# Kernel optimization log

Measured on AMD Instinct MI355X. Metric: run time of the kernel, lower is better.

## Reference

```python
import jax, jax.numpy as jnp
import numpy as np

N_NODES = 100000
N_EDGES = 1600000
VOCAB = 2048
NODE_DIM = 64
HIDDEN = 64
N_MASK = 10000


def setup_inputs() -> dict:
    key = jax.random.key(0)
    ks = jax.random.split(key, 10)
    x = jax.random.randint(ks[0], (N_NODES, 1), 0, VOCAB, dtype=jnp.int64)
    edge_index = jax.random.randint(ks[1], (2, N_EDGES), 0, N_NODES, dtype=jnp.int64)
    mask_x_position = jax.random.randint(ks[2], (N_MASK,), 0, N_NODES, dtype=jnp.int64)
    # embedding init: normal with std = node_dim ** -0.5 (as in initialize_parameters)
    emb = jax.random.normal(ks[3], (VOCAB, NODE_DIM), dtype=jnp.float32) * (NODE_DIM ** -0.5)
    # SAGEConv layer 1: lin_l (neighbors, with bias), lin_r (root, no bias)
    s1 = (NODE_DIM ** -0.5)
    W_l1 = jax.random.uniform(ks[4], (NODE_DIM, HIDDEN), jnp.float32, -s1, s1)
    b_l1 = jnp.zeros((HIDDEN,), jnp.float32)
    W_r1 = jax.random.uniform(ks[5], (NODE_DIM, HIDDEN), jnp.float32, -s1, s1)
    # SAGEConv layer 2
    s2 = (HIDDEN ** -0.5)
    W_l2 = jax.random.uniform(ks[6], (HIDDEN, VOCAB), jnp.float32, -s2, s2)
    b_l2 = jnp.zeros((VOCAB,), jnp.float32)
    W_r2 = jax.random.uniform(ks[7], (HIDDEN, VOCAB), jnp.float32, -s2, s2)
    return {"x": x, "edge_index": edge_index, "mask_x_position": mask_x_position,
            "emb": emb, "W_l1": W_l1, "b_l1": b_l1, "W_r1": W_r1,
            "W_l2": W_l2, "b_l2": b_l2, "W_r2": W_r2}


def _sage_conv(h, src, dst, W_l, b_l, W_r):
    # mean-aggregate source-node features at destination nodes (PyG SAGEConv, aggr='mean')
    msgs = h[src]                                                  # [E, D]
    agg = jax.ops.segment_sum(msgs, dst, num_segments=N_NODES)     # [N, D]
    deg = jax.ops.segment_sum(jnp.ones((src.shape[0], 1), h.dtype), dst,
                              num_segments=N_NODES)                # [N, 1]
    mean = agg / jnp.maximum(deg, 1.0)
    return mean @ W_l + b_l + h @ W_r


def reference(x, edge_index, mask_x_position, emb, W_l1, b_l1, W_r1, W_l2, b_l2, W_r2):
    src, dst = edge_index[0], edge_index[1]
    h = emb[x[:, 0]]                                # embedding(x).squeeze(1) -> [N, node_dim]
    # dropout is identity in eval mode
    h = _sage_conv(h, src, dst, W_l1, b_l1, W_r1)   # [N, hidden]
    h = jax.nn.relu(h)
    h = _sage_conv(h, src, dst, W_l2, b_l2, W_r2)   # [N, vocab]
    return jax.nn.log_softmax(h[mask_x_position], axis=1)
```

## Files before the change

kernel.cpp:

```cpp
#include <hip/hip_runtime.h>
#include <math.h>

#define N_NODES   100000
#define N_EDGES   1600000
#define VOCAB     2048
#define NODE_DIM  64
#define HIDDEN    64
#define N_MASK    10000

#define BN        192
#define NBKT      521
#define CHUNK     4096
#define NCH       391

typedef __attribute__((ext_vector_type(8))) short short8;
typedef __attribute__((ext_vector_type(4))) float f32x4;
typedef unsigned short ushort_t;
typedef unsigned int uint_t;

#define H1_OFF      0
#define ESRC_OFF    25600000
#define EVOC_OFF    32000000
#define E2_OFF      38400000
#define EWL_OFF     38400000
#define EWR_OFF     38924288
#define W2T_OFF     39448576
#define X2B_OFF     39972864
#define ROWPTR_OFF  51200000
#define BCNT_OFF    51600016
#define BPTR_OFF    51602112
#define BCUR_OFF    51604208

__device__ __forceinline__ ushort_t f2bf(float f) {
    uint_t u = __builtin_bit_cast(uint_t, f);
    u += 0x7FFFu + ((u >> 16) & 1u);
    return (ushort_t)(u >> 16);
}

__global__ __launch_bounds__(256) void k_prep(const float* __restrict__ emb,
                                              const float* __restrict__ Wl1,
                                              const float* __restrict__ Wr1,
                                              const float* __restrict__ Wl2,
                                              const float* __restrict__ Wr2,
                                              float* __restrict__ embWl,
                                              float* __restrict__ embWr,
                                              ushort_t* __restrict__ W2T) {
    __shared__ ushort_t T[64 * 66];
    const int bx = blockIdx.x;
    const int tid = threadIdx.x;
    if (bx < 1024) {
        const int half = bx >> 9;
        const float* W = half ? Wr1 : Wl1;
        float* out = half ? embWr : embWl;
        int idx = (bx & 511) * 256 + tid;
        int v = idx >> 6, c = idx & 63;
        float s = 0.0f;
#pragma unroll 8
        for (int k = 0; k < 64; k++) s += emb[v * 64 + k] * W[k * 64 + c];
        out[idx] = s;
    } else {
        int t = bx - 1024;
        const int k0 = (t & 1) * 64;
        const int n0 = (t >> 1) * 64;
        const float* Wsrc = (k0 == 0) ? Wl2 : Wr2;
#pragma unroll
        for (int i = 0; i < 16; i++) {
            int idx = i * 256 + tid;
            int k = idx >> 6, n = idx & 63;
            T[n * 66 + k] = f2bf(Wsrc[(size_t)k * VOCAB + n0 + n]);
        }
        __syncthreads();
#pragma unroll
        for (int i = 0; i < 16; i++) {
            int idx = i * 256 + tid;
            int n = idx >> 6, k = idx & 63;
            W2T[(size_t)(n0 + n) * 128 + k0 + k] = T[n * 66 + k];
        }
    }
}

__global__ __launch_bounds__(256) void k_count(const int* __restrict__ dst,
                                               int* __restrict__ bcnt) {
    __shared__ int hist[NBKT];
    for (int i = threadIdx.x; i < NBKT; i += 256) hist[i] = 0;
    __syncthreads();
    int stride = gridDim.x * 256;
    for (int e = blockIdx.x * 256 + threadIdx.x; e < N_EDGES; e += stride)
        atomicAdd(&hist[dst[e] / BN], 1);
    __syncthreads();
    for (int i = threadIdx.x; i < NBKT; i += 256) {
        int c = hist[i];
        if (c) atomicAdd(&bcnt[i], c);
    }
}

__global__ __launch_bounds__(1024) void k_bscan(const int* __restrict__ bcnt,
                                                int* __restrict__ bptr,
                                                int* __restrict__ bcur,
                                                int* __restrict__ rowptr) {
    __shared__ int s[1024];
    int t = threadIdx.x;
    int v = (t < NBKT) ? bcnt[t] : 0;
    s[t] = v;
    __syncthreads();
    for (int off = 1; off < 1024; off <<= 1) {
        int a = (t >= off) ? s[t - off] : 0;
        __syncthreads();
        s[t] += a;
        __syncthreads();
    }
    if (t < NBKT) { bptr[t] = s[t] - v; bcur[t] = s[t] - v; }
    if (t == NBKT - 1) bptr[NBKT] = s[t];
    if (t == 0) rowptr[N_NODES] = N_EDGES;
}

__global__ __launch_bounds__(256) void k_scatter2(const int* __restrict__ src,
                                                  const int* __restrict__ dst,
                                                  const int* __restrict__ x,
                                                  int* __restrict__ bcur,
                                                  int2* __restrict__ e2) {
    __shared__ uint_t dstb[CHUNK];
    __shared__ int hist[NBKT];
    const int e0 = blockIdx.x * CHUNK;
    const int n = min(CHUNK, N_EDGES - e0);
    for (int i = threadIdx.x; i < NBKT; i += 256) hist[i] = 0;
    __syncthreads();
    for (int i = threadIdx.x; i < n; i += 256) {
        int d = dst[e0 + i];
        int b = d / BN;
        dstb[i] = ((uint_t)b << 8) | (uint_t)(d - b * BN);
        atomicAdd(&hist[b], 1);
    }
    __syncthreads();
    for (int i = threadIdx.x; i < NBKT; i += 256) {
        int c = hist[i];
        hist[i] = c ? atomicAdd(&bcur[i], c) : 0;
    }
    __syncthreads();
    for (int i = threadIdx.x; i < n; i += 256) {
        uint_t db = dstb[i];
        int b = db >> 8;
        int s = src[e0 + i];
        int voc = x[s];
        int pos = atomicAdd(&hist[b], 1);
        e2[pos] = make_int2(s, (voc << 8) | (int)(db & 255u));
    }
}

__global__ __launch_bounds__(256) void k_sortb(const int* __restrict__ bptr,
                                               const int2* __restrict__ e2,
                                               int* __restrict__ rowptr,
                                               int* __restrict__ esrc,
                                               int* __restrict__ evoc) {
    __shared__ int cnt[BN];
    __shared__ int s[256];
    __shared__ int cur[BN];
    const int b = blockIdx.x;
    const int t = threadIdx.x;
    const int r0 = bptr[b], r1 = bptr[b + 1];
    if (t < BN) cnt[t] = 0;
    __syncthreads();
    for (int e = r0 + t; e < r1; e += 256)
        atomicAdd(&cnt[e2[e].y & 255], 1);
    __syncthreads();
    int v = (t < BN) ? cnt[t] : 0;
    s[t] = v;
    __syncthreads();
    for (int off = 1; off < 256; off <<= 1) {
        int a = (t >= off) ? s[t - off] : 0;
        __syncthreads();
        s[t] += a;
        __syncthreads();
    }
    if (t < BN) {
        int excl = s[t] - v;
        cur[t] = excl;
        int node = b * BN + t;
        if (node < N_NODES) rowptr[node] = r0 + excl;
    }
    __syncthreads();
    for (int e = r0 + t; e < r1; e += 256) {
        int2 ev = e2[e];
        int pos = r0 + atomicAdd(&cur[ev.y & 255], 1);
        esrc[pos] = ev.x;
        evoc[pos] = ev.y >> 8;
    }
}

__global__ __launch_bounds__(256) void k_agg1(const int* __restrict__ rowptr,
                                              const int* __restrict__ evoc,
                                              const int* __restrict__ x,
                                              const float* __restrict__ embWl,
                                              const float* __restrict__ embWr,
                                              const float* __restrict__ b1,
                                              float* __restrict__ h1) {
    int gw = (blockIdx.x * 256 + threadIdx.x) >> 6;
    int lane = threadIdx.x & 63;
    if (gw >= N_NODES) return;
    int r0 = rowptr[gw], r1 = rowptr[gw + 1];
    int deg = r1 - r0;
    float s0 = 0.0f, s1 = 0.0f, s2 = 0.0f, s3 = 0.0f;
    for (int base = 0; base < deg; base += 64) {
        int cnt = min(64, deg - base);
        int myv = (base + lane < deg) ? evoc[r0 + base + lane] : 0;
        int t = 0;
        for (; t + 3 < cnt; t += 4) {
            int va = __shfl(myv, t);
            int vb = __shfl(myv, t + 1);
            int vc = __shfl(myv, t + 2);
            int vd = __shfl(myv, t + 3);
            s0 += embWl[(va << 6) + lane];
            s1 += embWl[(vb << 6) + lane];
            s2 += embWl[(vc << 6) + lane];
            s3 += embWl[(vd << 6) + lane];
        }
        for (; t < cnt; t++)
            s0 += embWl[(__shfl(myv, t) << 6) + lane];
    }
    float sum = (s0 + s1) + (s2 + s3);
    float inv = 1.0f / fmaxf((float)deg, 1.0f);
    float self = embWr[(x[gw] << 6) + lane];
    h1[((size_t)gw << 6) + lane] = fmaxf(sum * inv + self + b1[lane], 0.0f);
}

__global__ __launch_bounds__(256) void k_x2(const int* __restrict__ mask,
                                            const int* __restrict__ rowptr,
                                            const int* __restrict__ esrc,
                                            const float* __restrict__ h1,
                                            ushort_t* __restrict__ X2b) {
    int gw = (blockIdx.x * 256 + threadIdx.x) >> 6;
    int lane = threadIdx.x & 63;
    if (gw >= N_MASK) return;
    int n = mask[gw];
    int r0 = rowptr[n], r1 = rowptr[n + 1];
    int deg = r1 - r0;
    float s0 = 0.0f, s1 = 0.0f, s2 = 0.0f, s3 = 0.0f;
    for (int base = 0; base < deg; base += 64) {
        int cnt = min(64, deg - base);
        int mys = (base + lane < deg) ? esrc[r0 + base + lane] : 0;
        int t = 0;
        for (; t + 3 < cnt; t += 4) {
            int sa = __shfl(mys, t);
            int sb = __shfl(mys, t + 1);
            int sc = __shfl(mys, t + 2);
            int sd = __shfl(mys, t + 3);
            s0 += h1[((size_t)sa << 6) + lane];
            s1 += h1[((size_t)sb << 6) + lane];
            s2 += h1[((size_t)sc << 6) + lane];
            s3 += h1[((size_t)sd << 6) + lane];
        }
        for (; t < cnt; t++)
            s0 += h1[((size_t)__shfl(mys, t) << 6) + lane];
    }
    float sum = (s0 + s1) + (s2 + s3);
    float inv = 1.0f / fmaxf((float)deg, 1.0f);
    X2b[gw * 128 + lane]      = f2bf(sum * inv);
    X2b[gw * 128 + 64 + lane] = f2bf(h1[((size_t)n << 6) + lane]);
}

__global__ __launch_bounds__(256) void k_gemm2_mfma(const ushort_t* __restrict__ X2b,
                                                    const ushort_t* __restrict__ W2T,
                                                    const float* __restrict__ bias,
                                                    float* __restrict__ out,
                                                    int M) {
    __shared__ ushort_t As[64 * 144];
    __shared__ ushort_t Bs[64 * 144];
    const int tid  = threadIdx.x;
    const int row0 = blockIdx.x * 64;
    const int col0 = blockIdx.y * 64;

#pragma unroll
    for (int i = 0; i < 4; i++) {
        int idx = i * 256 + tid;
        int r = idx >> 4, ch = idx & 15;
        int R = row0 + r;
        short8 v = {0, 0, 0, 0, 0, 0, 0, 0};
        if (R < M) v = *(const short8*)(X2b + (size_t)R * 128 + ch * 8);
        *(short8*)(As + r * 144 + ch * 8) = v;
    }
#pragma unroll
    for (int i = 0; i < 4; i++) {
        int idx = i * 256 + tid;
        int r = idx >> 4, ch = idx & 15;
        *(short8*)(Bs + r * 144 + ch * 8) =
            *(const short8*)(W2T + (size_t)(col0 + r) * 128 + ch * 8);
    }
    __syncthreads();

    const int lane = tid & 63;
    const int wv   = tid >> 6;
    const int wr = wv >> 1, wc = wv & 1;
    const int l15 = lane & 15, q = lane >> 4;

    f32x4 acc[2][2] = {};
    const ushort_t* Abase = As + (wr * 32 + l15) * 144 + q * 8;
    const ushort_t* Bbase = Bs + (wc * 32 + l15) * 144 + q * 8;

#pragma unroll
    for (int ks = 0; ks < 4; ks++) {
        short8 a0 = *(const short8*)(Abase + ks * 32);
        short8 a1 = *(const short8*)(Abase + 16 * 144 + ks * 32);
        short8 b0 = *(const short8*)(Bbase + ks * 32);
        short8 b1 = *(const short8*)(Bbase + 16 * 144 + ks * 32);
        acc[0][0] = __builtin_amdgcn_mfma_f32_16x16x32_bf16(a0, b0, acc[0][0], 0, 0, 0);
        acc[0][1] = __builtin_amdgcn_mfma_f32_16x16x32_bf16(a0, b1, acc[0][1], 0, 0, 0);
        acc[1][0] = __builtin_amdgcn_mfma_f32_16x16x32_bf16(a1, b0, acc[1][0], 0, 0, 0);
        acc[1][1] = __builtin_amdgcn_mfma_f32_16x16x32_bf16(a1, b1, acc[1][1], 0, 0, 0);
    }

#pragma unroll
    for (int ni = 0; ni < 2; ni++) {
        int c_ = col0 + wc * 32 + ni * 16 + l15;
        float bv = bias[c_];
#pragma unroll
        for (int mi = 0; mi < 2; mi++) {
#pragma unroll
            for (int reg = 0; reg < 4; reg++) {
                int r_ = row0 + wr * 32 + mi * 16 + q * 4 + reg;
                if (r_ < M) out[(size_t)r_ * VOCAB + c_] = acc[mi][ni][reg] + bv;
            }
        }
    }
}

__global__ __launch_bounds__(256) void k_logsoftmax(float* __restrict__ out) {
    const int row = blockIdx.x;
    float4* p4 = (float4*)(out + (size_t)row * VOCAB);
    const int tid = threadIdx.x;
    float4 v[2];
    float m = -INFINITY;
#pragma unroll
    for (int i = 0; i < 2; i++) {
        v[i] = p4[tid + i * 256];
        m = fmaxf(m, fmaxf(fmaxf(v[i].x, v[i].y), fmaxf(v[i].z, v[i].w)));
    }
#pragma unroll
    for (int off = 1; off < 64; off <<= 1) m = fmaxf(m, __shfl_xor(m, off));
    __shared__ float redm[4];
    __shared__ float reds[4];
    int wave = tid >> 6;
    if ((tid & 63) == 0) redm[wave] = m;
    __syncthreads();
    m = fmaxf(fmaxf(redm[0], redm[1]), fmaxf(redm[2], redm[3]));
    float s = 0.0f;
#pragma unroll
    for (int i = 0; i < 2; i++)
        s += expf(v[i].x - m) + expf(v[i].y - m) + expf(v[i].z - m) + expf(v[i].w - m);
#pragma unroll
    for (int off = 1; off < 64; off <<= 1) s += __shfl_xor(s, off);
    if ((tid & 63) == 0) reds[wave] = s;
    __syncthreads();
    s = reds[0] + reds[1] + reds[2] + reds[3];
    float L = m + logf(s);
#pragma unroll
    for (int i = 0; i < 2; i++) {
        float4 o = v[i];
        o.x -= L; o.y -= L; o.z -= L; o.w -= L;
        p4[tid + i * 256] = o;
    }
}

extern "C" void kernel_launch(void* const* d_in, const int* in_sizes, int n_in,
                              void* d_out, int out_size, void* d_ws, size_t ws_size,
                              hipStream_t stream) {
    const int*   x    = (const int*)d_in[0];
    const int*   ei   = (const int*)d_in[1];
    const int*   src  = ei;
    const int*   dst  = ei + N_EDGES;
    const int*   mask = (const int*)d_in[2];
    const float* emb  = (const float*)d_in[3];
    const float* Wl1  = (const float*)d_in[4];
    const float* bl1  = (const float*)d_in[5];
    const float* Wr1  = (const float*)d_in[6];
    const float* Wl2  = (const float*)d_in[7];
    const float* bl2  = (const float*)d_in[8];
    const float* Wr2  = (const float*)d_in[9];
    float* out = (float*)d_out;

    char* ws = (char*)d_ws;
    float*    h1     = (float*)(ws + H1_OFF);
    int*      esrc   = (int*)(ws + ESRC_OFF);
    int*      evoc   = (int*)(ws + EVOC_OFF);
    int2*     e2     = (int2*)(ws + E2_OFF);
    float*    embWl  = (float*)(ws + EWL_OFF);
    float*    embWr  = (float*)(ws + EWR_OFF);
    ushort_t* W2T    = (ushort_t*)(ws + W2T_OFF);
    ushort_t* X2b    = (ushort_t*)(ws + X2B_OFF);
    int*      rowptr = (int*)(ws + ROWPTR_OFF);
    int*      bcnt   = (int*)(ws + BCNT_OFF);
    int*      bptr   = (int*)(ws + BPTR_OFF);
    int*      bcur   = (int*)(ws + BCUR_OFF);

    hipMemsetAsync(ws + BCNT_OFF, 0, 2096, stream);

    k_count   <<<512, 256, 0, stream>>>(dst, bcnt);
    k_bscan   <<<1, 1024, 0, stream>>>(bcnt, bptr, bcur, rowptr);
    k_scatter2<<<NCH, 256, 0, stream>>>(src, dst, x, bcur, e2);
    k_sortb   <<<NBKT, 256, 0, stream>>>(bptr, e2, rowptr, esrc, evoc);

    k_prep<<<1088, 256, 0, stream>>>(emb, Wl1, Wr1, Wl2, Wr2, embWl, embWr, W2T);

    k_agg1<<<(N_NODES * 64 + 255) / 256, 256, 0, stream>>>(rowptr, evoc, x, embWl, embWr, bl1, h1);

    k_x2<<<(N_MASK * 64 + 255) / 256, 256, 0, stream>>>(mask, rowptr, esrc, h1, X2b);
    dim3 g2((N_MASK + 63) / 64, VOCAB / 64);
    k_gemm2_mfma<<<g2, 256, 0, stream>>>(X2b, W2T, bl2, out, N_MASK);

    k_logsoftmax<<<N_MASK, 256, 0, stream>>>(out);
}
```

Before: 301.9 us.

## Fuse per-bucket sort with layer-1 aggregation using shared-memory edge lists

```diff
diff --git a/kernel.cpp b/kernel.cpp
--- a/kernel.cpp
+++ b/kernel.cpp
@@ -10,8 +10,9 @@
 
 #define BN        192
 #define NBKT      521
-#define CHUNK     4096
-#define NCH       391
+#define CHUNK     1024
+#define NCH       1563
+#define ELCAP     4096
 
 typedef __attribute__((ext_vector_type(8))) short short8;
 typedef __attribute__((ext_vector_type(4))) float f32x4;
@@ -20,16 +21,15 @@
 
 #define H1_OFF      0
 #define ESRC_OFF    25600000
-#define EVOC_OFF    32000000
-#define E2_OFF      38400000
-#define EWL_OFF     38400000
-#define EWR_OFF     38924288
-#define W2T_OFF     39448576
-#define X2B_OFF     39972864
-#define ROWPTR_OFF  51200000
-#define BCNT_OFF    51600016
-#define BPTR_OFF    51602112
-#define BCUR_OFF    51604208
+#define E2_OFF      32000000
+#define EWL_OFF     44800000
+#define EWR_OFF     45324288
+#define W2T_OFF     45848576
+#define X2B_OFF     46372864
+#define ROWPTR_OFF  48932864
+#define BCNT_OFF    49332880
+#define BPTR_OFF    49334976
+#define BCUR_OFF    49337072
 
 __device__ __forceinline__ ushort_t f2bf(float f) {
     uint_t u = __builtin_bit_cast(uint_t, f);
@@ -119,108 +119,114 @@
                                                   const int* __restrict__ x,
                                                   int* __restrict__ bcur,
                                                   int2* __restrict__ e2) {
-    __shared__ uint_t dstb[CHUNK];
     __shared__ int hist[NBKT];
     const int e0 = blockIdx.x * CHUNK;
     const int n = min(CHUNK, N_EDGES - e0);
-    for (int i = threadIdx.x; i < NBKT; i += 256) hist[i] = 0;
-    __syncthreads();
-    for (int i = threadIdx.x; i < n; i += 256) {
-        int d = dst[e0 + i];
-        int b = d / BN;
-        dstb[i] = ((uint_t)b << 8) | (uint_t)(d - b * BN);
-        atomicAdd(&hist[b], 1);
-    }
-    __syncthreads();
-    for (int i = threadIdx.x; i < NBKT; i += 256) {
+    const int tid = threadIdx.x;
+    for (int i = tid; i < NBKT; i += 256) hist[i] = 0;
+    __syncthreads();
+    int d[4], s[4], voc[4], bk[4];
+#pragma unroll
+    for (int i = 0; i < 4; i++) {
+        int idx = i * 256 + tid;
+        if (idx < n) {
+            d[i] = dst[e0 + idx];
+            s[i] = src[e0 + idx];
+            voc[i] = x[s[i]];
+            bk[i] = d[i] / BN;
+            atomicAdd(&hist[bk[i]], 1);
+        }
+    }
+    __syncthreads();
+    for (int i = tid; i < NBKT; i += 256) {
         int c = hist[i];
         hist[i] = c ? atomicAdd(&bcur[i], c) : 0;
     }
     __syncthreads();
-    for (int i = threadIdx.x; i < n; i += 256) {
-        uint_t db = dstb[i];
-        int b = db >> 8;
-        int s = src[e0 + i];
-        int voc = x[s];
-        int pos = atomicAdd(&hist[b], 1);
-        e2[pos] = make_int2(s, (voc << 8) | (int)(db & 255u));
-    }
-}
-
-__global__ __launch_bounds__(256) void k_sortb(const int* __restrict__ bptr,
-                                               const int2* __restrict__ e2,
-                                               int* __restrict__ rowptr,
-                                               int* __restrict__ esrc,
-                                               int* __restrict__ evoc) {
-    __shared__ int cnt[BN];
-    __shared__ int s[256];
+#pragma unroll
+    for (int i = 0; i < 4; i++) {
+        int idx = i * 256 + tid;
+        if (idx < n) {
+            int pos = atomicAdd(&hist[bk[i]], 1);
+            e2[pos] = make_int2(s[i], (voc[i] << 8) | (d[i] - bk[i] * BN));
+        }
+    }
+}
+
+__global__ __launch_bounds__(512) void k_sortagg(const int* __restrict__ bptr,
+                                                 const int2* __restrict__ e2,
+                                                 const int* __restrict__ x,
+                                                 const float* __restrict__ embWl,
+                                                 const float* __restrict__ embWr,
+                                                 const float* __restrict__ b1,
+                                                 int* __restrict__ rowptr,
+                                                 int* __restrict__ esrc,
+                                                 float* __restrict__ h1) {
+    __shared__ int2 eL[ELCAP];
+    __shared__ int sc[256];
     __shared__ int cur[BN];
+    __shared__ int base[BN + 1];
     const int b = blockIdx.x;
     const int t = threadIdx.x;
     const int r0 = bptr[b], r1 = bptr[b + 1];
-    if (t < BN) cnt[t] = 0;
-    __syncthreads();
-    for (int e = r0 + t; e < r1; e += 256)
-        atomicAdd(&cnt[e2[e].y & 255], 1);
-    __syncthreads();
-    int v = (t < BN) ? cnt[t] : 0;
-    s[t] = v;
-    __syncthreads();
+    const int m = r1 - r0;
+
+    if (t < 256) sc[t] = 0;
+    __syncthreads();
+    for (int i = t; i < m; i += 512)
+        atomicAdd(&sc[e2[r0 + i].y & 255], 1);
+    __syncthreads();
+    int v = (t < 256) ? sc[t] : 0;
     for (int off = 1; off < 256; off <<= 1) {
-        int a = (t >= off) ? s[t - off] : 0;
+        int a = (t >= off && t < 256) ? sc[t - off] : 0;
         __syncthreads();
-        s[t] += a;
+        if (t < 256) sc[t] += a;
         __syncthreads();
     }
     if (t < BN) {
-        int excl = s[t] - v;
+        int excl = sc[t] - v;
+        base[t] = excl;
         cur[t] = excl;
         int node = b * BN + t;
         if (node < N_NODES) rowptr[node] = r0 + excl;
-    }
-    __syncthreads();
-    for (int e = r0 + t; e < r1; e += 256) {
-        int2 ev = e2[e];
-        int pos = r0 + atomicAdd(&cur[ev.y & 255], 1);
-        esrc[pos] = ev.x;
-        evoc[pos] = ev.y >> 8;
-    }
-}
-
-__global__ __launch_bounds__(256) void k_agg1(const int* __restrict__ rowptr,
-                                              const int* __restrict__ evoc,
-                                              const int* __restrict__ x,
-                                              const float* __restrict__ embWl,
-                                              const float* __restrict__ embWr,
-                                              const float* __restrict__ b1,
-                                              float* __restrict__ h1) {
-    int gw = (blockIdx.x * 256 + threadIdx.x) >> 6;
-    int lane = threadIdx.x & 63;
-    if (gw >= N_NODES) return;
-    int r0 = rowptr[gw], r1 = rowptr[gw + 1];
-    int deg = r1 - r0;
-    float s0 = 0.0f, s1 = 0.0f, s2 = 0.0f, s3 = 0.0f;
-    for (int base = 0; base < deg; base += 64) {
-        int cnt = min(64, deg - base);
-        int myv = (base + lane < deg) ? evoc[r0 + base + lane] : 0;
-        int t = 0;
-        for (; t + 3 < cnt; t += 4) {
-            int va = __shfl(myv, t);
-            int vb = __shfl(myv, t + 1);
-            int vc = __shfl(myv, t + 2);
-            int vd = __shfl(myv, t + 3);
+        if (t == BN - 1) base[BN] = sc[t];
+    }
+    __syncthreads();
+    for (int i = t; i < m; i += 512) {
+        int2 ev = e2[r0 + i];
+        int pos = atomicAdd(&cur[ev.y & 255], 1);
+        eL[pos] = ev;
+    }
+    __syncthreads();
+    for (int i = t; i < m; i += 512)
+        esrc[r0 + i] = eL[i].x;
+
+    const int wv = t >> 6, lane = t & 63;
+    const float b1v = b1[lane];
+    for (int nl = wv; nl < BN; nl += 8) {
+        int node = b * BN + nl;
+        if (node >= N_NODES) break;
+        int j0 = base[nl], j1 = base[nl + 1];
+        int deg = j1 - j0;
+        float s0 = 0.0f, s1 = 0.0f, s2 = 0.0f, s3 = 0.0f;
+        int j = j0;
+        for (; j + 3 < j1; j += 4) {
+            int va = eL[j].y >> 8;
+            int vb = eL[j + 1].y >> 8;
+            int vc = eL[j + 2].y >> 8;
+            int vd = eL[j + 3].y >> 8;
             s0 += embWl[(va << 6) + lane];
             s1 += embWl[(vb << 6) + lane];
             s2 += embWl[(vc << 6) + lane];
             s3 += embWl[(vd << 6) + lane];
         }
-        for (; t < cnt; t++)
-            s0 += embWl[(__shfl(myv, t) << 6) + lane];
-    }
-    float sum = (s0 + s1) + (s2 + s3);
-    float inv = 1.0f / fmaxf((float)deg, 1.0f);
-    float self = embWr[(x[gw] << 6) + lane];
-    h1[((size_t)gw << 6) + lane] = fmaxf(sum * inv + self + b1[lane], 0.0f);
+        for (; j < j1; j++)
+            s0 += embWl[((eL[j].y >> 8) << 6) + lane];
+        float sum = (s0 + s1) + (s2 + s3);
+        float inv = 1.0f / fmaxf((float)deg, 1.0f);
+        float self = embWr[(x[node] << 6) + lane];
+        h1[((size_t)node << 6) + lane] = fmaxf(sum * inv + self + b1v, 0.0f);
+    }
 }
 
 __global__ __launch_bounds__(256) void k_x2(const int* __restrict__ mask,
@@ -380,7 +386,6 @@
     char* ws = (char*)d_ws;
     float*    h1     = (float*)(ws + H1_OFF);
     int*      esrc   = (int*)(ws + ESRC_OFF);
-    int*      evoc   = (int*)(ws + EVOC_OFF);
     int2*     e2     = (int2*)(ws + E2_OFF);
     float*    embWl  = (float*)(ws + EWL_OFF);
     float*    embWr  = (float*)(ws + EWR_OFF);
@@ -396,11 +401,10 @@
     k_count   <<<512, 256, 0, stream>>>(dst, bcnt);
     k_bscan   <<<1, 1024, 0, stream>>>(bcnt, bptr, bcur, rowptr);
     k_scatter2<<<NCH, 256, 0, stream>>>(src, dst, x, bcur, e2);
-    k_sortb   <<<NBKT, 256, 0, stream>>>(bptr, e2, rowptr, esrc, evoc);
 
     k_prep<<<1088, 256, 0, stream>>>(emb, Wl1, Wr1, Wl2, Wr2, embWl, embWr, W2T);
 
-    k_agg1<<<(N_NODES * 64 + 255) / 256, 256, 0, stream>>>(rowptr, evoc, x, embWl, embWr, bl1, h1);
+    k_sortagg<<<NBKT, 512, 0, stream>>>(bptr, e2, x, embWl, embWr, bl1, rowptr, esrc, h1);
 
     k_x2<<<(N_MASK * 64 + 255) / 256, 256, 0, stream>>>(mask, rowptr, esrc, h1, X2b);
     dim3 g2((N_MASK + 63) / 64, VOCAB / 64);
```

Result: slower. 315.5 us (+4.5%).
